# Performance work log

Measured on AMD Instinct MI355X. Metric: run time of the kernel, lower is better.

## Reference

```python
import jax, jax.numpy as jnp
import numpy as np

B, C, H, W = 8, 64, 256, 256


def setup_inputs() -> dict:
    key = jax.random.key(0)
    ks = jax.random.split(key, 7)
    return {
        "x": jax.random.normal(ks[0], (B, C, H, W), dtype=jnp.float32),
        "query_w": jax.random.normal(ks[1], (C, W, W), dtype=jnp.float32),
        "key_w": jax.random.normal(ks[2], (C, W, W), dtype=jnp.float32),
        "var_w": jax.random.normal(ks[3], (C, W, W), dtype=jnp.float32),
        "query_b": jax.random.normal(ks[4], (C, H, W), dtype=jnp.float32),
        "key_b": jax.random.normal(ks[5], (C, H, W), dtype=jnp.float32),
        "var_b": jax.random.normal(ks[6], (C, H, W), dtype=jnp.float32),
    }


def reference(x, query_w, key_w, var_w, query_b, key_b, var_b):
    # mode == 'horizontal': per-channel right-matmul over the W axis.
    # x: [B,C,H,W], *_w: [C,W,W] (broadcast over batch), *_b: [C,H,W].
    q = jnp.einsum("bchw,cwv->bchv", x, query_w) + query_b
    k = jnp.einsum("bchw,cwv->bchv", x, key_w) + key_b
    v = jnp.einsum("bchw,cwv->bchv", x, var_w) + var_b
    return jax.nn.softmax(q * k, axis=-1) * v
```

## Files before the change

kernel.cpp:

```cpp
#include <hip/hip_runtime.h>
#include <math.h>


#define Bn 8
#define Cn 64
#define Hn 256
#define Wn 256

typedef _Float16 f16x8 __attribute__((ext_vector_type(8)));
typedef _Float16 f16x4 __attribute__((ext_vector_type(4)));
typedef float    f32x16 __attribute__((ext_vector_type(16)));

#define MFMA(a, b, c) __builtin_amdgcn_mfma_f32_32x32x16_f16((a), (b), (c), 0, 0, 0)

#define LDS_ALO 4096
#define LDS_B   8192
#define LDS_SM  40960

__global__ __launch_bounds__(512, 2) void axile_attn_mfma2(
    const float* __restrict__ x,
    const float* __restrict__ wq,
    const float* __restrict__ wk,
    const float* __restrict__ wv,
    const float* __restrict__ bq,
    const float* __restrict__ bk,
    const float* __restrict__ bv,
    float* __restrict__ out)
{
    __shared__ __align__(16) char lds[44032];

    const int tid  = threadIdx.x;
    const int wave = tid >> 6;
    const int lane = tid & 63;
    const int h    = lane >> 5;
    const int l31  = lane & 31;

    const int blk = blockIdx.x;
    const int c   = blk & 63;
    const int j   = blk >> 6;
    const int b   = j >> 1;
    const int h0  = (j & 1) * 128;

    const int mrow = wave >> 2;
    const int ncol = wave & 3;

    const float* xbase = x + ((size_t)(b * Cn + c) * Hn + h0) * Wn;
    const float* w_q = wq + (size_t)c * Wn * Wn;
    const float* w_k = wk + (size_t)c * Wn * Wn;
    const float* w_v = wv + (size_t)c * Wn * Wn;

    const int kg    = tid >> 8;
    const int n     = tid & 255;
    const int ntW   = n >> 5;
    const int lcW   = (kg << 5) | (n & 31);
    const int am    = tid >> 2;
    const int akq   = tid & 3;
    const int amt   = am >> 5;
    const int alc   = ((akq >> 1) << 5) | (am & 31);
    const int aboff = (akq & 1) * 8;

    f32x16 accq[2][2], acck[2][2];
#pragma unroll
    for (int mt = 0; mt < 2; ++mt)
#pragma unroll
        for (int nt = 0; nt < 2; ++nt)
#pragma unroll
            for (int r = 0; r < 16; ++r) {
                accq[mt][nt][r] = 0.f;
                acck[mt][nt][r] = 0.f;
            }

    for (int kt = 0; kt < 16; ++kt) {
        const int k0 = kt * 16;
        __syncthreads();
        {
            char* dst = lds + LDS_B + ntW * 1024 + lcW * 16;
#pragma unroll
            for (int mat = 0; mat < 2; ++mat) {
                const float* Wp = mat ? w_k : w_q;
                float w8[8];
#pragma unroll
                for (int r = 0; r < 8; ++r)
                    w8[r] = Wp[(size_t)(k0 + kg * 8 + r) * Wn + n];
                f16x8 hi8, lo8;
#pragma unroll
                for (int r = 0; r < 8; ++r) {
                    _Float16 hv = (_Float16)w8[r];
                    hi8[r] = hv;
                    lo8[r] = (_Float16)(w8[r] - (float)hv);
                }
                *(f16x8*)(dst + (mat * 2) * 8192) = hi8;
                *(f16x8*)(dst + (mat * 2 + 1) * 8192) = lo8;
            }
        }
        {
            const float4 xx = *(const float4*)(xbase + (size_t)am * Wn + k0 + akq * 4);
            f16x4 hi4, lo4;
            _Float16 t0 = (_Float16)xx.x; hi4[0] = t0; lo4[0] = (_Float16)(xx.x - (float)t0);
            _Float16 t1 = (_Float16)xx.y; hi4[1] = t1; lo4[1] = (_Float16)(xx.y - (float)t1);
            _Float16 t2 = (_Float16)xx.z; hi4[2] = t2; lo4[2] = (_Float16)(xx.z - (float)t2);
            _Float16 t3 = (_Float16)xx.w; hi4[3] = t3; lo4[3] = (_Float16)(xx.w - (float)t3);
            *(f16x4*)(lds + amt * 1024 + alc * 16 + aboff) = hi4;
            *(f16x4*)(lds + LDS_ALO + amt * 1024 + alc * 16 + aboff) = lo4;
        }
        __syncthreads();

        f16x8 ah[2], al[2];
#pragma unroll
        for (int mt = 0; mt < 2; ++mt) {
            const int mtile = mrow * 2 + mt;
            ah[mt] = *(const f16x8*)(lds + mtile * 1024 + lane * 16);
            al[mt] = *(const f16x8*)(lds + LDS_ALO + mtile * 1024 + lane * 16);
        }
#pragma unroll
        for (int nt = 0; nt < 2; ++nt) {
            const int ntile = ncol * 2 + nt;
            const char* bb = lds + LDS_B + ntile * 1024 + lane * 16;
            f16x8 bqh = *(const f16x8*)(bb + 0 * 8192);
            f16x8 bql = *(const f16x8*)(bb + 1 * 8192);
            f16x8 bkh = *(const f16x8*)(bb + 2 * 8192);
            f16x8 bkl = *(const f16x8*)(bb + 3 * 8192);
#pragma unroll
            for (int mt = 0; mt < 2; ++mt) {
                accq[mt][nt] = MFMA(ah[mt], bqh, accq[mt][nt]);
                accq[mt][nt] = MFMA(al[mt], bqh, accq[mt][nt]);
                accq[mt][nt] = MFMA(ah[mt], bql, accq[mt][nt]);
                acck[mt][nt] = MFMA(ah[mt], bkh, acck[mt][nt]);
                acck[mt][nt] = MFMA(al[mt], bkh, acck[mt][nt]);
                acck[mt][nt] = MFMA(ah[mt], bkl, acck[mt][nt]);
            }
        }
    }

    float* part    = (float*)(lds + LDS_SM);
    float* combmax = (float*)(lds + LDS_SM + 2048);
    float* combsum = (float*)(lds + LDS_SM + 2560);

#pragma unroll
    for (int mt = 0; mt < 2; ++mt)
#pragma unroll
        for (int nt = 0; nt < 2; ++nt)
#pragma unroll
            for (int r = 0; r < 16; ++r) {
                const int rl = (r & 3) + 8 * (r >> 2) + 4 * h;
                const int hh = h0 + mrow * 64 + mt * 32 + rl;
                const int vv = ncol * 64 + nt * 32 + l31;
                const size_t bidx = ((size_t)c * Hn + hh) * Wn + vv;
                const float qv = accq[mt][nt][r] + bq[bidx];
                const float kv = acck[mt][nt][r] + bk[bidx];
                accq[mt][nt][r] = qv * kv;
            }

#pragma unroll
    for (int mt = 0; mt < 2; ++mt)
#pragma unroll
        for (int r = 0; r < 16; ++r) {
            float m2 = fmaxf(accq[mt][0][r], accq[mt][1][r]);
#pragma unroll
            for (int off = 16; off > 0; off >>= 1)
                m2 = fmaxf(m2, __shfl_xor(m2, off, 64));
            if ((lane & 15) == r && ((lane >> 4) & 1) == mt) {
                const int rl  = (r & 3) + 8 * (r >> 2) + 4 * h;
                const int row = mrow * 64 + mt * 32 + rl;
                part[row * 4 + ncol] = m2;
            }
        }
    __syncthreads();
    if (tid < 128)
        combmax[tid] = fmaxf(fmaxf(part[tid * 4 + 0], part[tid * 4 + 1]),
                             fmaxf(part[tid * 4 + 2], part[tid * 4 + 3]));
    __syncthreads();

#pragma unroll
    for (int mt = 0; mt < 2; ++mt)
#pragma unroll
        for (int r = 0; r < 16; ++r) {
            const int rl  = (r & 3) + 8 * (r >> 2) + 4 * h;
            const int row = mrow * 64 + mt * 32 + rl;
            const float mx = combmax[row];
            const float e0 = __expf(accq[mt][0][r] - mx);
            const float e1 = __expf(accq[mt][1][r] - mx);
            accq[mt][0][r] = e0;
            accq[mt][1][r] = e1;
            float ps = e0 + e1;
#pragma unroll
            for (int off = 16; off > 0; off >>= 1)
                ps += __shfl_xor(ps, off, 64);
            if ((lane & 15) == r && ((lane >> 4) & 1) == mt)
                part[row * 4 + ncol] = ps;
        }
    __syncthreads();
    if (tid < 128)
        combsum[tid] = (part[tid * 4 + 0] + part[tid * 4 + 1]) +
                       (part[tid * 4 + 2] + part[tid * 4 + 3]);

    f32x16 accv[2][2];
#pragma unroll
    for (int mt = 0; mt < 2; ++mt)
#pragma unroll
        for (int nt = 0; nt < 2; ++nt)
#pragma unroll
            for (int r = 0; r < 16; ++r)
                accv[mt][nt][r] = 0.f;

    for (int kt = 0; kt < 16; ++kt) {
        const int k0 = kt * 16;
        __syncthreads();
        {
            char* dst = lds + LDS_B + ntW * 1024 + lcW * 16;
            float w8[8];
#pragma unroll
            for (int r = 0; r < 8; ++r)
                w8[r] = w_v[(size_t)(k0 + kg * 8 + r) * Wn + n];
            f16x8 hi8;
#pragma unroll
            for (int r = 0; r < 8; ++r)
                hi8[r] = (_Float16)w8[r];
            *(f16x8*)dst = hi8;
        }
        {
            const float4 xx = *(const float4*)(xbase + (size_t)am * Wn + k0 + akq * 4);
            f16x4 hi4;
            hi4[0] = (_Float16)xx.x;
            hi4[1] = (_Float16)xx.y;
            hi4[2] = (_Float16)xx.z;
            hi4[3] = (_Float16)xx.w;
            *(f16x4*)(lds + amt * 1024 + alc * 16 + aboff) = hi4;
        }
        __syncthreads();

        f16x8 ah[2];
#pragma unroll
        for (int mt = 0; mt < 2; ++mt)
            ah[mt] = *(const f16x8*)(lds + (mrow * 2 + mt) * 1024 + lane * 16);
#pragma unroll
        for (int nt = 0; nt < 2; ++nt) {
            const int ntile = ncol * 2 + nt;
            f16x8 bvh = *(const f16x8*)(lds + LDS_B + ntile * 1024 + lane * 16);
#pragma unroll
            for (int mt = 0; mt < 2; ++mt)
                accv[mt][nt] = MFMA(ah[mt], bvh, accv[mt][nt]);
        }
    }

    float* obase = out + ((size_t)(b * Cn + c) * Hn) * Wn;
#pragma unroll
    for (int mt = 0; mt < 2; ++mt)
#pragma unroll
        for (int r = 0; r < 16; ++r) {
            const int rl  = (r & 3) + 8 * (r >> 2) + 4 * h;
            const int row = mrow * 64 + mt * 32 + rl;
            const float inv = 1.0f / combsum[row];
            const int hh = h0 + row;
#pragma unroll
            for (int nt = 0; nt < 2; ++nt) {
                const int vv = ncol * 64 + nt * 32 + l31;
                const size_t bidx = ((size_t)c * Hn + hh) * Wn + vv;
                const float vx = accv[mt][nt][r] + bv[bidx];
                obase[(size_t)hh * Wn + vv] = accq[mt][nt][r] * vx * inv;
            }
        }
}

extern "C" void kernel_launch(void* const* d_in, const int* in_sizes, int n_in,
                              void* d_out, int out_size, void* d_ws, size_t ws_size,
                              hipStream_t stream) {
    (void)in_sizes; (void)n_in; (void)out_size; (void)d_ws; (void)ws_size;
    const float* x  = (const float*)d_in[0];
    const float* wq = (const float*)d_in[1];
    const float* wk = (const float*)d_in[2];
    const float* wv = (const float*)d_in[3];
    const float* bq = (const float*)d_in[4];
    const float* bk = (const float*)d_in[5];
    const float* bv = (const float*)d_in[6];
    float* out = (float*)d_out;

    dim3 grid(Bn * 2 * Cn);
    dim3 block(512);
    hipLaunchKernelGGL(axile_attn_mfma2, grid, block, 0, stream,
                       x, wq, wk, wv, bq, bk, bv, out);
}
```

Measured before the change: 547.4 us.

## Shrink row tile to 64 rows with 256-thread blocks and more CTAs

Result: faster. 534.0 us (-2.5%).

```diff
diff --git a/kernel.cpp b/kernel.cpp
--- a/kernel.cpp
+++ b/kernel.cpp
@@ -13,11 +13,11 @@
 
 #define MFMA(a, b, c) __builtin_amdgcn_mfma_f32_32x32x16_f16((a), (b), (c), 0, 0, 0)
 
-#define LDS_ALO 4096
-#define LDS_B   8192
-#define LDS_SM  40960
-
-__global__ __launch_bounds__(512, 2) void axile_attn_mfma2(
+#define LDS_ALO 2048
+#define LDS_B   4096
+#define LDS_SM  36864
+
+__global__ __launch_bounds__(256, 2) void axile_attn_mfma3(
     const float* __restrict__ x,
     const float* __restrict__ wq,
     const float* __restrict__ wk,
@@ -27,10 +27,10 @@
     const float* __restrict__ bv,
     float* __restrict__ out)
 {
-    __shared__ __align__(16) char lds[44032];
+    __shared__ __align__(16) char lds[38400];
 
     const int tid  = threadIdx.x;
-    const int wave = tid >> 6;
+    const int ncol = tid >> 6;
     const int lane = tid & 63;
     const int h    = lane >> 5;
     const int l31  = lane & 31;
@@ -38,21 +38,17 @@
     const int blk = blockIdx.x;
     const int c   = blk & 63;
     const int j   = blk >> 6;
-    const int b   = j >> 1;
-    const int h0  = (j & 1) * 128;
-
-    const int mrow = wave >> 2;
-    const int ncol = wave & 3;
+    const int b   = j >> 2;
+    const int h0  = (j & 3) * 64;
 
     const float* xbase = x + ((size_t)(b * Cn + c) * Hn + h0) * Wn;
     const float* w_q = wq + (size_t)c * Wn * Wn;
     const float* w_k = wk + (size_t)c * Wn * Wn;
     const float* w_v = wv + (size_t)c * Wn * Wn;
 
-    const int kg    = tid >> 8;
-    const int n     = tid & 255;
-    const int ntW   = n >> 5;
-    const int lcW   = (kg << 5) | (n & 31);
+    const int n    = tid;
+    const int ntW  = n >> 5;
+    const int nl   = n & 31;
     const int am    = tid >> 2;
     const int akq   = tid & 3;
     const int amt   = am >> 5;
@@ -73,24 +69,27 @@
     for (int kt = 0; kt < 16; ++kt) {
         const int k0 = kt * 16;
         __syncthreads();
-        {
-            char* dst = lds + LDS_B + ntW * 1024 + lcW * 16;
-#pragma unroll
-            for (int mat = 0; mat < 2; ++mat) {
-                const float* Wp = mat ? w_k : w_q;
-                float w8[8];
-#pragma unroll
-                for (int r = 0; r < 8; ++r)
-                    w8[r] = Wp[(size_t)(k0 + kg * 8 + r) * Wn + n];
+#pragma unroll
+        for (int mat = 0; mat < 2; ++mat) {
+            const float* Wp = mat ? w_k : w_q;
+            float w16[16];
+#pragma unroll
+            for (int r = 0; r < 16; ++r)
+                w16[r] = Wp[(size_t)(k0 + r) * Wn + n];
+            char* dplane = lds + LDS_B + (mat * 2) * 8192 + ntW * 1024;
+#pragma unroll
+            for (int h2 = 0; h2 < 2; ++h2) {
                 f16x8 hi8, lo8;
 #pragma unroll
-                for (int r = 0; r < 8; ++r) {
-                    _Float16 hv = (_Float16)w8[r];
-                    hi8[r] = hv;
-                    lo8[r] = (_Float16)(w8[r] - (float)hv);
+                for (int e = 0; e < 8; ++e) {
+                    const float wv_ = w16[h2 * 8 + e];
+                    _Float16 hv = (_Float16)wv_;
+                    hi8[e] = hv;
+                    lo8[e] = (_Float16)(wv_ - (float)hv);
                 }
-                *(f16x8*)(dst + (mat * 2) * 8192) = hi8;
-                *(f16x8*)(dst + (mat * 2 + 1) * 8192) = lo8;
+                const int fo = ((h2 << 5) | nl) * 16;
+                *(f16x8*)(dplane + fo) = hi8;
+                *(f16x8*)(dplane + 8192 + fo) = lo8;
             }
         }
         {
@@ -108,9 +107,8 @@
         f16x8 ah[2], al[2];
 #pragma unroll
         for (int mt = 0; mt < 2; ++mt) {
-            const int mtile = mrow * 2 + mt;
-            ah[mt] = *(const f16x8*)(lds + mtile * 1024 + lane * 16);
-            al[mt] = *(const f16x8*)(lds + LDS_ALO + mtile * 1024 + lane * 16);
+            ah[mt] = *(const f16x8*)(lds + mt * 1024 + lane * 16);
+            al[mt] = *(const f16x8*)(lds + LDS_ALO + mt * 1024 + lane * 16);
         }
 #pragma unroll
         for (int nt = 0; nt < 2; ++nt) {
@@ -133,8 +131,8 @@
     }
 
     float* part    = (float*)(lds + LDS_SM);
-    float* combmax = (float*)(lds + LDS_SM + 2048);
-    float* combsum = (float*)(lds + LDS_SM + 2560);
+    float* combmax = (float*)(lds + LDS_SM + 1024);
+    float* combsum = (float*)(lds + LDS_SM + 1280);
 
 #pragma unroll
     for (int mt = 0; mt < 2; ++mt)
@@ -143,7 +141,7 @@
 #pragma unroll
             for (int r = 0; r < 16; ++r) {
                 const int rl = (r & 3) + 8 * (r >> 2) + 4 * h;
-                const int hh = h0 + mrow * 64 + mt * 32 + rl;
+                const int hh = h0 + mt * 32 + rl;
                 const int vv = ncol * 64 + nt * 32 + l31;
                 const size_t bidx = ((size_t)c * Hn + hh) * Wn + vv;
                 const float qv = accq[mt][nt][r] + bq[bidx];
@@ -161,12 +159,12 @@
                 m2 = fmaxf(m2, __shfl_xor(m2, off, 64));
             if ((lane & 15) == r && ((lane >> 4) & 1) == mt) {
                 const int rl  = (r & 3) + 8 * (r >> 2) + 4 * h;
-                const int row = mrow * 64 + mt * 32 + rl;
+                const int row = mt * 32 + rl;
                 part[row * 4 + ncol] = m2;
             }
         }
     __syncthreads();
-    if (tid < 128)
+    if (tid < 64)
         combmax[tid] = fmaxf(fmaxf(part[tid * 4 + 0], part[tid * 4 + 1]),
                              fmaxf(part[tid * 4 + 2], part[tid * 4 + 3]));
     __syncthreads();
@@ -176,7 +174,7 @@
 #pragma unroll
         for (int r = 0; r < 16; ++r) {
             const int rl  = (r & 3) + 8 * (r >> 2) + 4 * h;
-            const int row = mrow * 64 + mt * 32 + rl;
+            const int row = mt * 32 + rl;
             const float mx = combmax[row];
             const float e0 = __expf(accq[mt][0][r] - mx);
             const float e1 = __expf(accq[mt][1][r] - mx);
@@ -190,7 +188,7 @@
                 part[row * 4 + ncol] = ps;
         }
     __syncthreads();
-    if (tid < 128)
+    if (tid < 64)
         combsum[tid] = (part[tid * 4 + 0] + part[tid * 4 + 1]) +
                        (part[tid * 4 + 2] + part[tid * 4 + 3]);
 
@@ -207,16 +205,19 @@
         const int k0 = kt * 16;
         __syncthreads();
         {
-            char* dst = lds + LDS_B + ntW * 1024 + lcW * 16;
-            float w8[8];
-#pragma unroll
-            for (int r = 0; r < 8; ++r)
-                w8[r] = w_v[(size_t)(k0 + kg * 8 + r) * Wn + n];
-            f16x8 hi8;
-#pragma unroll
-            for (int r = 0; r < 8; ++r)
-                hi8[r] = (_Float16)w8[r];
-            *(f16x8*)dst = hi8;
+            float w16[16];
+#pragma unroll
+            for (int r = 0; r < 16; ++r)
+                w16[r] = w_v[(size_t)(k0 + r) * Wn + n];
+            char* dplane = lds + LDS_B + ntW * 1024;
+#pragma unroll
+            for (int h2 = 0; h2 < 2; ++h2) {
+                f16x8 hi8;
+#pragma unroll
+                for (int e = 0; e < 8; ++e)
+                    hi8[e] = (_Float16)w16[h2 * 8 + e];
+                *(f16x8*)(dplane + ((h2 << 5) | nl) * 16) = hi8;
+            }
         }
         {
             const float4 xx = *(const float4*)(xbase + (size_t)am * Wn + k0 + akq * 4);
@@ -232,7 +233,7 @@
         f16x8 ah[2];
 #pragma unroll
         for (int mt = 0; mt < 2; ++mt)
-            ah[mt] = *(const f16x8*)(lds + (mrow * 2 + mt) * 1024 + lane * 16);
+            ah[mt] = *(const f16x8*)(lds + mt * 1024 + lane * 16);
 #pragma unroll
         for (int nt = 0; nt < 2; ++nt) {
             const int ntile = ncol * 2 + nt;
@@ -249,7 +250,7 @@
 #pragma unroll
         for (int r = 0; r < 16; ++r) {
             const int rl  = (r & 3) + 8 * (r >> 2) + 4 * h;
-            const int row = mrow * 64 + mt * 32 + rl;
+            const int row = mt * 32 + rl;
             const float inv = 1.0f / combsum[row];
             const int hh = h0 + row;
 #pragma unroll
@@ -275,8 +276,8 @@
     const float* bv = (const float*)d_in[6];
     float* out = (float*)d_out;
 
-    dim3 grid(Bn * 2 * Cn);
-    dim3 block(512);
-    hipLaunchKernelGGL(axile_attn_mfma2, grid, block, 0, stream,
+    dim3 grid(Bn * 4 * Cn);
+    dim3 block(256);
+    hipLaunchKernelGGL(axile_attn_mfma3, grid, block, 0, stream,
                        x, wq, wk, wv, bq, bk, bv, out);
 }
```
